# Performance work log

Measured on AMD Instinct MI355X. Metric: run time of the kernel, lower is better.

Reference implementation:

```python
import jax, jax.numpy as jnp
import numpy as np

EPS = 1e-5


def conv1d(x, w, b):
    # x: (B, C_in, S), w: (C_out, C_in, K), 'same' padding = K//2
    pad = w.shape[-1] // 2
    y = jax.lax.conv_general_dilated(
        x, w, window_strides=(1,), padding=[(pad, pad)],
        dimension_numbers=("NCH", "OIH", "NCH"))
    return y + b[None, :, None]


def layer_norm(x, g, b):
    m = jnp.mean(x, axis=-1, keepdims=True)
    v = jnp.var(x, axis=-1, keepdims=True)
    return (x - m) * jax.lax.rsqrt(v + EPS) * g + b


def duration_predict(x, conv1_w, conv1_b, conv2_w, conv2_b,
                     ln1_g, ln1_b, ln2_g, ln2_b, lin_w, lin_b):
    # x: (B, S, C)
    out = conv1d(jnp.swapaxes(x, -2, -1), conv1_w, conv1_b)          # (B, F, S)
    out = jax.nn.relu(layer_norm(jnp.swapaxes(out, -2, -1), ln1_g, ln1_b))  # (B, S, F)
    out = conv1d(jnp.swapaxes(out, -2, -1), conv2_w, conv2_b)        # (B, F, S)
    out = jax.nn.relu(layer_norm(jnp.swapaxes(out, -2, -1), ln2_g, ln2_b))  # (B, S, F)
    out = jax.nn.relu(out @ lin_w.T + lin_b)                          # (B, S, 1)
    return jnp.squeeze(out, -1)                                       # (B, S)


def setup_inputs() -> dict:
    key = jax.random.key(0)
    ks = jax.random.split(key, 6)
    B, S, C = 16, 1024, 256
    F_, K = 256, 3
    inp = {
        "x": jax.random.normal(ks[0], (B, S, C), dtype=jnp.float32),
        "target": jax.random.uniform(ks[1], (B, S), dtype=jnp.float32),
        "conv1_w": jax.random.normal(ks[2], (F_, C, K), dtype=jnp.float32) * 0.02,
        "conv1_b": jnp.zeros((F_,), dtype=jnp.float32),
        "conv2_w": jax.random.normal(ks[3], (F_, F_, K), dtype=jnp.float32) * 0.02,
        "conv2_b": jnp.zeros((F_,), dtype=jnp.float32),
        "ln1_g": jnp.ones((F_,), dtype=jnp.float32),
        "ln1_b": jnp.zeros((F_,), dtype=jnp.float32),
        "ln2_g": jnp.ones((F_,), dtype=jnp.float32),
        "ln2_b": jnp.zeros((F_,), dtype=jnp.float32),
        "lin_w": jax.random.normal(ks[4], (1, F_), dtype=jnp.float32) * 0.02,
        "lin_b": jnp.zeros((1,), dtype=jnp.float32),
    }
    return inp


def reference(x, target, conv1_w, conv1_b, conv2_w, conv2_b,
              ln1_g, ln1_b, ln2_g, ln2_b, lin_w, lin_b):
    reg_len = duration_predict(x, conv1_w, conv1_b, conv2_w, conv2_b,
                               ln1_g, ln1_b, ln2_g, ln2_b, lin_w, lin_b)
    # Faithful to the original: max_len uses exp(target), the mask uses round(target).
    # max_len is data-dependent -> computed from concrete target (host-side, like the original).
    max_len = int(np.round(float(jnp.max(jnp.sum(jnp.exp(target), axis=-1)))))
    d = jnp.round(target)                 # (B, S) integer-valued durations (banker's rounding, like Python round)
    fin = jnp.cumsum(d, axis=-1)          # (B, S) end offsets
    start = fin - d                       # (B, S) start offsets
    t = jnp.arange(max_len, dtype=target.dtype)  # (T,)
    mask = ((t[None, None, :] >= start[..., None]) &
            (t[None, None, :] < fin[..., None])).astype(x.dtype)  # (B, S, T)
    # x.transpose @ mask -> (B, C, T) -> transpose -> (B, T, C)
    expanded = jnp.einsum("bsc,bst->btc", x, mask)
    return expanded, reg_len
```

## Files before the change

kernel.cpp:

```cpp
#include <hip/hip_runtime.h>
#include <hip/hip_bf16.h>

using frag_ab = __attribute__((ext_vector_type(8))) short;
using frag_cd = __attribute__((ext_vector_type(4))) float;

#define SLEN 1024
#define CDIM 256
#define KTOT 768

static __device__ __forceinline__ short f2bf(float f) {
    __hip_bfloat16 h = __float2bfloat16(f);
    return *reinterpret_cast<short*>(&h);
}

__global__ __launch_bounds__(1024) void scan_scatter_kernel(
    const float* __restrict__ target, int* __restrict__ src, int T)
{
    const int b = blockIdx.x;
    const int tid = threadIdx.x;

    for (int i = tid; i < T; i += 1024) src[b * T + i] = -1;

    const float tv = target[b * SLEN + tid];
    const int d = (int)rintf(tv);

    const int lane = tid & 63;
    const int wid = tid >> 6;
    int v = d;
#pragma unroll
    for (int off = 1; off < 64; off <<= 1) {
        int n = __shfl_up(v, off);
        if (lane >= off) v += n;
    }
    __shared__ int waveSum[16];
    if (lane == 63) waveSum[wid] = v;
    __syncthreads();
    if (tid < 16) {
        int wv = waveSum[tid];
#pragma unroll
        for (int off = 1; off < 16; off <<= 1) {
            int n = __shfl_up(wv, off);
            if (tid >= off) wv += n;
        }
        waveSum[tid] = wv;
    }
    __syncthreads();
    const int fin = v + (wid > 0 ? waveSum[wid - 1] : 0);
    const int start = fin - d;
    for (int t = start; t < fin; ++t)
        if (t >= 0 && t < T) src[b * T + t] = tid;
}

__global__ __launch_bounds__(256) void expand_kernel(
    const float* __restrict__ x, const int* __restrict__ src,
    float* __restrict__ out, int T)
{
    const int row = blockIdx.x * 4 + (threadIdx.x >> 6);
    const int lane = threadIdx.x & 63;
    const int nrows = 16 * T;
    if (row >= nrows) return;
    const int b = row / T;
    const int s = src[row];
    float4 val = make_float4(0.f, 0.f, 0.f, 0.f);
    if (s >= 0)
        val = *(const float4*)(x + ((size_t)(b * SLEN + s)) * CDIM + lane * 4);
    *(float4*)(out + (size_t)row * CDIM + lane * 4) = val;
}

__global__ __launch_bounds__(256) void repack_w(
    const float* __restrict__ w, __hip_bfloat16* __restrict__ bt)
{
    const int f = blockIdx.y;
    const int K = blockIdx.x * 256 + threadIdx.x;
    const int k3 = K >> 8;
    const int c = K & 255;
    bt[f * KTOT + K] = __float2bfloat16(w[f * KTOT + c * 3 + k3]);
}

template <int MODE>
__global__ __launch_bounds__(512) void conv_mfma(
    const void* __restrict__ in_,
    const __hip_bfloat16* __restrict__ bt,
    const float* __restrict__ bias,
    const float* __restrict__ gamma,
    const float* __restrict__ beta,
    void* __restrict__ out_,
    const float* __restrict__ lw,
    const float* __restrict__ lb)
{
    __shared__ __align__(16) unsigned char ldsA[66 * 512];
    __shared__ float red[64][8][2];
    __shared__ float stats[64][2];

    const int tid = threadIdx.x;
    const int b = blockIdx.y;
    const int s0 = blockIdx.x * 64;

    if (MODE == 0) {
        const float* xin = (const float*)in_ + (size_t)b * SLEN * CDIM;
        for (int ii = tid; ii < 66 * 32; ii += 512) {
            const int r = ii >> 5, cc = ii & 31;
            const int s = s0 + r - 1;
            frag_ab v = {0, 0, 0, 0, 0, 0, 0, 0};
            if (s >= 0 && s < SLEN) {
                const float4* p = (const float4*)(xin + (size_t)s * CDIM + cc * 8);
                const float4 q0 = p[0], q1 = p[1];
                v[0] = f2bf(q0.x); v[1] = f2bf(q0.y); v[2] = f2bf(q0.z); v[3] = f2bf(q0.w);
                v[4] = f2bf(q1.x); v[5] = f2bf(q1.y); v[6] = f2bf(q1.z); v[7] = f2bf(q1.w);
            }
            *(frag_ab*)(ldsA + r * 512 + ((cc * 16) ^ ((r & 7) << 4))) = v;
        }
    } else {
        const __hip_bfloat16* yin = (const __hip_bfloat16*)in_ + (size_t)b * SLEN * CDIM;
        for (int ii = tid; ii < 66 * 32; ii += 512) {
            const int r = ii >> 5, cc = ii & 31;
            const int s = s0 + r - 1;
            frag_ab v = {0, 0, 0, 0, 0, 0, 0, 0};
            if (s >= 0 && s < SLEN)
                v = *(const frag_ab*)(yin + (size_t)s * CDIM + cc * 8);
            *(frag_ab*)(ldsA + r * 512 + ((cc * 16) ^ ((r & 7) << 4))) = v;
        }
    }
    __syncthreads();

    const int lane = tid & 63;
    const int wid = tid >> 6;
    const int l15 = lane & 15;
    const int lk = lane >> 4;
    const int fbase = wid * 32;

    frag_cd acc[4][2];
#pragma unroll
    for (int mf = 0; mf < 4; ++mf) {
        acc[mf][0] = {0.f, 0.f, 0.f, 0.f};
        acc[mf][1] = {0.f, 0.f, 0.f, 0.f};
    }

    const __hip_bfloat16* bt0 = bt + (size_t)(fbase + l15) * KTOT + lk * 8;
    const __hip_bfloat16* bt1 = bt0 + 16 * KTOT;

#pragma unroll
    for (int kk = 0; kk < 24; ++kk) {
        const int k3 = kk >> 3;
        const int colbyte = (kk & 7) * 64 + lk * 16;
        const frag_ab bb0 = *(const frag_ab*)(bt0 + kk * 32);
        const frag_ab bb1 = *(const frag_ab*)(bt1 + kk * 32);
        frag_ab a[4];
#pragma unroll
        for (int mf = 0; mf < 4; ++mf) {
            const int r = mf * 16 + l15 + k3;
            a[mf] = *(const frag_ab*)(ldsA + r * 512 + (colbyte ^ ((r & 7) << 4)));
        }
#pragma unroll
        for (int mf = 0; mf < 4; ++mf) {
            acc[mf][0] = __builtin_amdgcn_mfma_f32_16x16x32_bf16(a[mf], bb0, acc[mf][0], 0, 0, 0);
            acc[mf][1] = __builtin_amdgcn_mfma_f32_16x16x32_bf16(a[mf], bb1, acc[mf][1], 0, 0, 0);
        }
    }

    const float bias0 = bias[fbase + l15];
    const float bias1 = bias[fbase + 16 + l15];
#pragma unroll
    for (int mf = 0; mf < 4; ++mf) {
#pragma unroll
        for (int j = 0; j < 4; ++j) {
            acc[mf][0][j] += bias0;
            acc[mf][1][j] += bias1;
            float p = acc[mf][0][j] + acc[mf][1][j];
            float q = acc[mf][0][j] * acc[mf][0][j] + acc[mf][1][j] * acc[mf][1][j];
#pragma unroll
            for (int m = 1; m < 16; m <<= 1) {
                p += __shfl_xor(p, m);
                q += __shfl_xor(q, m);
            }
            if (l15 == 0) {
                const int row = mf * 16 + lk * 4 + j;
                red[row][wid][0] = p;
                red[row][wid][1] = q;
            }
        }
    }
    __syncthreads();
    if (tid < 64) {
        float s = 0.f, q = 0.f;
#pragma unroll
        for (int wv = 0; wv < 8; ++wv) { s += red[tid][wv][0]; q += red[tid][wv][1]; }
        const float mean = s * (1.f / 256.f);
        const float var = q * (1.f / 256.f) - mean * mean;
        stats[tid][0] = mean;
        stats[tid][1] = rsqrtf(var + 1e-5f);
    }
    __syncthreads();

    const float g0 = gamma[fbase + l15], g1 = gamma[fbase + 16 + l15];
    const float be0 = beta[fbase + l15], be1 = beta[fbase + 16 + l15];

    if (MODE == 0) {
#pragma unroll
        for (int mf = 0; mf < 4; ++mf) {
#pragma unroll
            for (int j = 0; j < 4; ++j) {
                const int row = mf * 16 + lk * 4 + j;
                const float mean = stats[row][0], rs = stats[row][1];
                const float v0 = fmaxf((acc[mf][0][j] - mean) * rs * g0 + be0, 0.f);
                const float v1 = fmaxf((acc[mf][1][j] - mean) * rs * g1 + be1, 0.f);
                *(short*)(ldsA + row * 512 + (fbase + l15) * 2) = f2bf(v0);
                *(short*)(ldsA + row * 512 + (fbase + 16 + l15) * 2) = f2bf(v1);
            }
        }
        __syncthreads();
        __hip_bfloat16* yout = (__hip_bfloat16*)out_ + ((size_t)b * SLEN + s0) * CDIM;
        for (int ii = tid; ii < 64 * 32; ii += 512) {
            const int r = ii >> 5, cc = ii & 31;
            *(frag_ab*)(yout + (size_t)r * CDIM + cc * 8) =
                *(const frag_ab*)(ldsA + r * 512 + cc * 16);
        }
    } else {
        const float lw0 = lw[fbase + l15], lw1 = lw[fbase + 16 + l15];
#pragma unroll
        for (int mf = 0; mf < 4; ++mf) {
#pragma unroll
            for (int j = 0; j < 4; ++j) {
                const int row = mf * 16 + lk * 4 + j;
                const float mean = stats[row][0], rs = stats[row][1];
                const float v0 = fmaxf((acc[mf][0][j] - mean) * rs * g0 + be0, 0.f);
                const float v1 = fmaxf((acc[mf][1][j] - mean) * rs * g1 + be1, 0.f);
                float p = v0 * lw0 + v1 * lw1;
#pragma unroll
                for (int m = 1; m < 16; m <<= 1) p += __shfl_xor(p, m);
                if (l15 == 0) red[row][wid][0] = p;
            }
        }
        __syncthreads();
        if (tid < 64) {
            float s = 0.f;
#pragma unroll
            for (int wv = 0; wv < 8; ++wv) s += red[tid][wv][0];
            ((float*)out_)[b * SLEN + s0 + tid] = fmaxf(s + lb[0], 0.f);
        }
    }
}

extern "C" void kernel_launch(void* const* d_in, const int* in_sizes, int n_in,
                              void* d_out, int out_size, void* d_ws, size_t ws_size,
                              hipStream_t stream)
{
    const float* x       = (const float*)d_in[0];
    const float* target  = (const float*)d_in[1];
    const float* conv1_w = (const float*)d_in[2];
    const float* conv1_b = (const float*)d_in[3];
    const float* conv2_w = (const float*)d_in[4];
    const float* conv2_b = (const float*)d_in[5];
    const float* ln1_g   = (const float*)d_in[6];
    const float* ln1_b   = (const float*)d_in[7];
    const float* ln2_g   = (const float*)d_in[8];
    const float* ln2_b   = (const float*)d_in[9];
    const float* lin_w   = (const float*)d_in[10];
    const float* lin_b   = (const float*)d_in[11];

    const int B = 16, S = 1024, C = 256;
    const int T = (out_size - B * S) / (B * C);

    float* expanded = (float*)d_out;
    float* reg_len  = (float*)d_out + (size_t)B * T * C;

    unsigned char* ws = (unsigned char*)d_ws;
    __hip_bfloat16* y1  = (__hip_bfloat16*)ws;
    __hip_bfloat16* bt1 = (__hip_bfloat16*)(ws + 8388608);
    __hip_bfloat16* bt2 = (__hip_bfloat16*)(ws + 8388608 + 393216);
    int* src = (int*)(ws + 8388608 + 2 * 393216);

    scan_scatter_kernel<<<B, 1024, 0, stream>>>(target, src, T);
    repack_w<<<dim3(3, 256), 256, 0, stream>>>(conv1_w, bt1);
    repack_w<<<dim3(3, 256), 256, 0, stream>>>(conv2_w, bt2);

    conv_mfma<0><<<dim3(16, 16), 512, 0, stream>>>(
        x, bt1, conv1_b, ln1_g, ln1_b, y1, nullptr, nullptr);

    expand_kernel<<<(B * T + 3) / 4, 256, 0, stream>>>(x, src, expanded, T);

    conv_mfma<1><<<dim3(16, 16), 512, 0, stream>>>(
        y1, bt2, conv2_b, ln2_g, ln2_b, reg_len, lin_w, lin_b);
}
```

Before: 62.91 us.

## Fuse both conv+layernorm stages into one kernel with halo recompute

Merges the two conv_mfma launches into a single kernel. Each block loads a 68-row x tile (two halo rows each side), computes conv1+LN1+ReLU for 66 rows into LDS, then runs conv2+LN2+linear directly from LDS. This removes the bf16 intermediate round trip through global memory and one kernel launch, at the cost of recomputing the halo rows, more LDS per block and more registers. The two weight-repack launches are also merged into one.

New measurement: 57.07 us. -9.3%, faster.

```diff
diff --git a/kernel.cpp b/kernel.cpp
--- a/kernel.cpp
+++ b/kernel.cpp
@@ -67,59 +67,50 @@
     *(float4*)(out + (size_t)row * CDIM + lane * 4) = val;
 }
 
-__global__ __launch_bounds__(256) void repack_w(
-    const float* __restrict__ w, __hip_bfloat16* __restrict__ bt)
+__global__ __launch_bounds__(256) void repack_w2(
+    const float* __restrict__ w1, __hip_bfloat16* __restrict__ bt1,
+    const float* __restrict__ w2, __hip_bfloat16* __restrict__ bt2)
 {
     const int f = blockIdx.y;
-    const int K = blockIdx.x * 256 + threadIdx.x;
+    const int which = blockIdx.x / 3;
+    const int K = (blockIdx.x % 3) * 256 + threadIdx.x;
     const int k3 = K >> 8;
     const int c = K & 255;
+    const float* w = which ? w2 : w1;
+    __hip_bfloat16* bt = which ? bt2 : bt1;
     bt[f * KTOT + K] = __float2bfloat16(w[f * KTOT + c * 3 + k3]);
 }
 
-template <int MODE>
-__global__ __launch_bounds__(512) void conv_mfma(
-    const void* __restrict__ in_,
-    const __hip_bfloat16* __restrict__ bt,
-    const float* __restrict__ bias,
-    const float* __restrict__ gamma,
-    const float* __restrict__ beta,
-    void* __restrict__ out_,
-    const float* __restrict__ lw,
-    const float* __restrict__ lb)
-{
-    __shared__ __align__(16) unsigned char ldsA[66 * 512];
-    __shared__ float red[64][8][2];
-    __shared__ float stats[64][2];
+__global__ __launch_bounds__(512) void fused_conv(
+    const float* __restrict__ x,
+    const __hip_bfloat16* __restrict__ bt1,
+    const __hip_bfloat16* __restrict__ bt2,
+    const float* __restrict__ cb1, const float* __restrict__ g1, const float* __restrict__ be1,
+    const float* __restrict__ cb2, const float* __restrict__ g2, const float* __restrict__ be2,
+    const float* __restrict__ lw, const float* __restrict__ lb,
+    float* __restrict__ reg_len)
+{
+    __shared__ __align__(16) unsigned char xt[82 * 512];
+    __shared__ __align__(16) unsigned char yt[66 * 512];
+    __shared__ float red[66][8][2];
+    __shared__ float stats[66][2];
 
     const int tid = threadIdx.x;
     const int b = blockIdx.y;
     const int s0 = blockIdx.x * 64;
 
-    if (MODE == 0) {
-        const float* xin = (const float*)in_ + (size_t)b * SLEN * CDIM;
-        for (int ii = tid; ii < 66 * 32; ii += 512) {
-            const int r = ii >> 5, cc = ii & 31;
-            const int s = s0 + r - 1;
-            frag_ab v = {0, 0, 0, 0, 0, 0, 0, 0};
-            if (s >= 0 && s < SLEN) {
-                const float4* p = (const float4*)(xin + (size_t)s * CDIM + cc * 8);
-                const float4 q0 = p[0], q1 = p[1];
-                v[0] = f2bf(q0.x); v[1] = f2bf(q0.y); v[2] = f2bf(q0.z); v[3] = f2bf(q0.w);
-                v[4] = f2bf(q1.x); v[5] = f2bf(q1.y); v[6] = f2bf(q1.z); v[7] = f2bf(q1.w);
-            }
-            *(frag_ab*)(ldsA + r * 512 + ((cc * 16) ^ ((r & 7) << 4))) = v;
-        }
-    } else {
-        const __hip_bfloat16* yin = (const __hip_bfloat16*)in_ + (size_t)b * SLEN * CDIM;
-        for (int ii = tid; ii < 66 * 32; ii += 512) {
-            const int r = ii >> 5, cc = ii & 31;
-            const int s = s0 + r - 1;
-            frag_ab v = {0, 0, 0, 0, 0, 0, 0, 0};
-            if (s >= 0 && s < SLEN)
-                v = *(const frag_ab*)(yin + (size_t)s * CDIM + cc * 8);
-            *(frag_ab*)(ldsA + r * 512 + ((cc * 16) ^ ((r & 7) << 4))) = v;
-        }
+    const float* xin = x + (size_t)b * SLEN * CDIM;
+    for (int ii = tid; ii < 68 * 32; ii += 512) {
+        const int r = ii >> 5, cc = ii & 31;
+        const int s = s0 - 2 + r;
+        frag_ab v = {0, 0, 0, 0, 0, 0, 0, 0};
+        if (s >= 0 && s < SLEN) {
+            const float4* p = (const float4*)(xin + (size_t)s * CDIM + cc * 8);
+            const float4 q0 = p[0], q1 = p[1];
+            v[0] = f2bf(q0.x); v[1] = f2bf(q0.y); v[2] = f2bf(q0.z); v[3] = f2bf(q0.w);
+            v[4] = f2bf(q1.x); v[5] = f2bf(q1.y); v[6] = f2bf(q1.z); v[7] = f2bf(q1.w);
+        }
+        *(frag_ab*)(xt + r * 512 + ((cc * 16) ^ ((r & 7) << 4))) = v;
     }
     __syncthreads();
 
@@ -129,59 +120,62 @@
     const int lk = lane >> 4;
     const int fbase = wid * 32;
 
-    frag_cd acc[4][2];
-#pragma unroll
-    for (int mf = 0; mf < 4; ++mf) {
-        acc[mf][0] = {0.f, 0.f, 0.f, 0.f};
-        acc[mf][1] = {0.f, 0.f, 0.f, 0.f};
-    }
-
-    const __hip_bfloat16* bt0 = bt + (size_t)(fbase + l15) * KTOT + lk * 8;
-    const __hip_bfloat16* bt1 = bt0 + 16 * KTOT;
-
-#pragma unroll
-    for (int kk = 0; kk < 24; ++kk) {
-        const int k3 = kk >> 3;
-        const int colbyte = (kk & 7) * 64 + lk * 16;
-        const frag_ab bb0 = *(const frag_ab*)(bt0 + kk * 32);
-        const frag_ab bb1 = *(const frag_ab*)(bt1 + kk * 32);
-        frag_ab a[4];
-#pragma unroll
-        for (int mf = 0; mf < 4; ++mf) {
-            const int r = mf * 16 + l15 + k3;
-            a[mf] = *(const frag_ab*)(ldsA + r * 512 + (colbyte ^ ((r & 7) << 4)));
-        }
-#pragma unroll
-        for (int mf = 0; mf < 4; ++mf) {
-            acc[mf][0] = __builtin_amdgcn_mfma_f32_16x16x32_bf16(a[mf], bb0, acc[mf][0], 0, 0, 0);
-            acc[mf][1] = __builtin_amdgcn_mfma_f32_16x16x32_bf16(a[mf], bb1, acc[mf][1], 0, 0, 0);
-        }
-    }
-
-    const float bias0 = bias[fbase + l15];
-    const float bias1 = bias[fbase + 16 + l15];
-#pragma unroll
-    for (int mf = 0; mf < 4; ++mf) {
-#pragma unroll
-        for (int j = 0; j < 4; ++j) {
-            acc[mf][0][j] += bias0;
-            acc[mf][1][j] += bias1;
-            float p = acc[mf][0][j] + acc[mf][1][j];
-            float q = acc[mf][0][j] * acc[mf][0][j] + acc[mf][1][j] * acc[mf][1][j];
-#pragma unroll
-            for (int m = 1; m < 16; m <<= 1) {
-                p += __shfl_xor(p, m);
-                q += __shfl_xor(q, m);
-            }
-            if (l15 == 0) {
-                const int row = mf * 16 + lk * 4 + j;
-                red[row][wid][0] = p;
-                red[row][wid][1] = q;
-            }
-        }
-    }
-    __syncthreads();
-    if (tid < 64) {
+    frag_cd acc1[5][2];
+#pragma unroll
+    for (int mf = 0; mf < 5; ++mf) {
+        acc1[mf][0] = {0.f, 0.f, 0.f, 0.f};
+        acc1[mf][1] = {0.f, 0.f, 0.f, 0.f};
+    }
+    {
+        const __hip_bfloat16* p0 = bt1 + (size_t)(fbase + l15) * KTOT + lk * 8;
+        const __hip_bfloat16* p1 = p0 + 16 * KTOT;
+#pragma unroll
+        for (int kk = 0; kk < 24; ++kk) {
+            const int k3 = kk >> 3;
+            const int colbyte = (kk & 7) * 64 + lk * 16;
+            const frag_ab bb0 = *(const frag_ab*)(p0 + kk * 32);
+            const frag_ab bb1 = *(const frag_ab*)(p1 + kk * 32);
+            frag_ab a[5];
+#pragma unroll
+            for (int mf = 0; mf < 5; ++mf) {
+                const int r = mf * 16 + l15 + k3;
+                a[mf] = *(const frag_ab*)(xt + r * 512 + (colbyte ^ ((r & 7) << 4)));
+            }
+#pragma unroll
+            for (int mf = 0; mf < 5; ++mf) {
+                acc1[mf][0] = __builtin_amdgcn_mfma_f32_16x16x32_bf16(a[mf], bb0, acc1[mf][0], 0, 0, 0);
+                acc1[mf][1] = __builtin_amdgcn_mfma_f32_16x16x32_bf16(a[mf], bb1, acc1[mf][1], 0, 0, 0);
+            }
+        }
+    }
+
+    {
+        const float bias0 = cb1[fbase + l15];
+        const float bias1 = cb1[fbase + 16 + l15];
+#pragma unroll
+        for (int mf = 0; mf < 5; ++mf) {
+#pragma unroll
+            for (int j = 0; j < 4; ++j) {
+                acc1[mf][0][j] += bias0;
+                acc1[mf][1][j] += bias1;
+                float p = acc1[mf][0][j] + acc1[mf][1][j];
+                float q = acc1[mf][0][j] * acc1[mf][0][j] + acc1[mf][1][j] * acc1[mf][1][j];
+#pragma unroll
+                for (int m = 1; m < 16; m <<= 1) {
+                    p += __shfl_xor(p, m);
+                    q += __shfl_xor(q, m);
+                }
+                const bool valid = (mf < 4) || (lk == 0 && j < 2);
+                if (l15 == 0 && valid) {
+                    const int yr = mf * 16 + lk * 4 + j;
+                    red[yr][wid][0] = p;
+                    red[yr][wid][1] = q;
+                }
+            }
+        }
+    }
+    __syncthreads();
+    if (tid < 66) {
         float s = 0.f, q = 0.f;
 #pragma unroll
         for (int wv = 0; wv < 8; ++wv) { s += red[tid][wv][0]; q += red[tid][wv][1]; }
@@ -192,52 +186,130 @@
     }
     __syncthreads();
 
-    const float g0 = gamma[fbase + l15], g1 = gamma[fbase + 16 + l15];
-    const float be0 = beta[fbase + l15], be1 = beta[fbase + 16 + l15];
-
-    if (MODE == 0) {
+    {
+        const float ga0 = g1[fbase + l15], ga1 = g1[fbase + 16 + l15];
+        const float bb0 = be1[fbase + l15], bb1 = be1[fbase + 16 + l15];
+        const int c0b = (fbase + l15) * 2;
+        const int c1b = (fbase + 16 + l15) * 2;
+#pragma unroll
+        for (int mf = 0; mf < 5; ++mf) {
+#pragma unroll
+            for (int j = 0; j < 4; ++j) {
+                const bool valid = (mf < 4) || (lk == 0 && j < 2);
+                if (valid) {
+                    const int yr = mf * 16 + lk * 4 + j;
+                    const float mean = stats[yr][0], rs = stats[yr][1];
+                    const float v0 = fmaxf((acc1[mf][0][j] - mean) * rs * ga0 + bb0, 0.f);
+                    const float v1 = fmaxf((acc1[mf][1][j] - mean) * rs * ga1 + bb1, 0.f);
+                    const int sw = (yr & 7) << 4;
+                    *(short*)(yt + yr * 512 + (c0b ^ sw)) = f2bf(v0);
+                    *(short*)(yt + yr * 512 + (c1b ^ sw)) = f2bf(v1);
+                }
+            }
+        }
+    }
+    __syncthreads();
+    if (blockIdx.x == 0 && tid < 32) {
+        frag_ab z = {0, 0, 0, 0, 0, 0, 0, 0};
+        *(frag_ab*)(yt + (tid * 16)) = z;
+    }
+    if (blockIdx.x == 15 && tid >= 64 && tid < 96) {
+        frag_ab z = {0, 0, 0, 0, 0, 0, 0, 0};
+        const int cc = tid - 64;
+        *(frag_ab*)(yt + 65 * 512 + ((cc * 16) ^ ((65 & 7) << 4))) = z;
+    }
+    __syncthreads();
+
+    frag_cd acc2[4][2];
+#pragma unroll
+    for (int mf = 0; mf < 4; ++mf) {
+        acc2[mf][0] = {0.f, 0.f, 0.f, 0.f};
+        acc2[mf][1] = {0.f, 0.f, 0.f, 0.f};
+    }
+    {
+        const __hip_bfloat16* p0 = bt2 + (size_t)(fbase + l15) * KTOT + lk * 8;
+        const __hip_bfloat16* p1 = p0 + 16 * KTOT;
+#pragma unroll
+        for (int kk = 0; kk < 24; ++kk) {
+            const int k3 = kk >> 3;
+            const int colbyte = (kk & 7) * 64 + lk * 16;
+            const frag_ab bb0 = *(const frag_ab*)(p0 + kk * 32);
+            const frag_ab bb1 = *(const frag_ab*)(p1 + kk * 32);
+            frag_ab a[4];
+#pragma unroll
+            for (int mf = 0; mf < 4; ++mf) {
+                const int r = mf * 16 + l15 + k3;
+                a[mf] = *(const frag_ab*)(yt + r * 512 + (colbyte ^ ((r & 7) << 4)));
+            }
+#pragma unroll
+            for (int mf = 0; mf < 4; ++mf) {
+                acc2[mf][0] = __builtin_amdgcn_mfma_f32_16x16x32_bf16(a[mf], bb0, acc2[mf][0], 0, 0, 0);
+                acc2[mf][1] = __builtin_amdgcn_mfma_f32_16x16x32_bf16(a[mf], bb1, acc2[mf][1], 0, 0, 0);
+            }
+        }
+    }
+
+    {
+        const float bias0 = cb2[fbase + l15];
+        const float bias1 = cb2[fbase + 16 + l15];
+#pragma unroll
+        for (int mf = 0; mf < 4; ++mf) {
+#pragma unroll
+            for (int j = 0; j < 4; ++j) {
+                acc2[mf][0][j] += bias0;
+                acc2[mf][1][j] += bias1;
+                float p = acc2[mf][0][j] + acc2[mf][1][j];
+                float q = acc2[mf][0][j] * acc2[mf][0][j] + acc2[mf][1][j] * acc2[mf][1][j];
+#pragma unroll
+                for (int m = 1; m < 16; m <<= 1) {
+                    p += __shfl_xor(p, m);
+                    q += __shfl_xor(q, m);
+                }
+                if (l15 == 0) {
+                    const int row = mf * 16 + lk * 4 + j;
+                    red[row][wid][0] = p;
+                    red[row][wid][1] = q;
+                }
+            }
+        }
+    }
+    __syncthreads();
+    if (tid < 64) {
+        float s = 0.f, q = 0.f;
+#pragma unroll
+        for (int wv = 0; wv < 8; ++wv) { s += red[tid][wv][0]; q += red[tid][wv][1]; }
+        const float mean = s * (1.f / 256.f);
+        const float var = q * (1.f / 256.f) - mean * mean;
+        stats[tid][0] = mean;
+        stats[tid][1] = rsqrtf(var + 1e-5f);
+    }
+    __syncthreads();
+
+    {
+        const float ga0 = g2[fbase + l15], ga1 = g2[fbase + 16 + l15];
+        const float bb0 = be2[fbase + l15], bb1 = be2[fbase + 16 + l15];
+        const float lw0 = lw[fbase + l15], lw1 = lw[fbase + 16 + l15];
 #pragma unroll
         for (int mf = 0; mf < 4; ++mf) {
 #pragma unroll
             for (int j = 0; j < 4; ++j) {
                 const int row = mf * 16 + lk * 4 + j;
                 const float mean = stats[row][0], rs = stats[row][1];
-                const float v0 = fmaxf((acc[mf][0][j] - mean) * rs * g0 + be0, 0.f);
-                const float v1 = fmaxf((acc[mf][1][j] - mean) * rs * g1 + be1, 0.f);
-                *(short*)(ldsA + row * 512 + (fbase + l15) * 2) = f2bf(v0);
-                *(short*)(ldsA + row * 512 + (fbase + 16 + l15) * 2) = f2bf(v1);
-            }
-        }
-        __syncthreads();
-        __hip_bfloat16* yout = (__hip_bfloat16*)out_ + ((size_t)b * SLEN + s0) * CDIM;
-        for (int ii = tid; ii < 64 * 32; ii += 512) {
-            const int r = ii >> 5, cc = ii & 31;
-            *(frag_ab*)(yout + (size_t)r * CDIM + cc * 8) =
-                *(const frag_ab*)(ldsA + r * 512 + cc * 16);
-        }
-    } else {
-        const float lw0 = lw[fbase + l15], lw1 = lw[fbase + 16 + l15];
-#pragma unroll
-        for (int mf = 0; mf < 4; ++mf) {
-#pragma unroll
-            for (int j = 0; j < 4; ++j) {
-                const int row = mf * 16 + lk * 4 + j;
-                const float mean = stats[row][0], rs = stats[row][1];
-                const float v0 = fmaxf((acc[mf][0][j] - mean) * rs * g0 + be0, 0.f);
-                const float v1 = fmaxf((acc[mf][1][j] - mean) * rs * g1 + be1, 0.f);
+                const float v0 = fmaxf((acc2[mf][0][j] - mean) * rs * ga0 + bb0, 0.f);
+                const float v1 = fmaxf((acc2[mf][1][j] - mean) * rs * ga1 + bb1, 0.f);
                 float p = v0 * lw0 + v1 * lw1;
 #pragma unroll
                 for (int m = 1; m < 16; m <<= 1) p += __shfl_xor(p, m);
                 if (l15 == 0) red[row][wid][0] = p;
             }
         }
-        __syncthreads();
-        if (tid < 64) {
-            float s = 0.f;
-#pragma unroll
-            for (int wv = 0; wv < 8; ++wv) s += red[tid][wv][0];
-            ((float*)out_)[b * SLEN + s0 + tid] = fmaxf(s + lb[0], 0.f);
-        }
+    }
+    __syncthreads();
+    if (tid < 64) {
+        float s = 0.f;
+#pragma unroll
+        for (int wv = 0; wv < 8; ++wv) s += red[tid][wv][0];
+        reg_len[b * SLEN + s0 + tid] = fmaxf(s + lb[0], 0.f);
     }
 }
 
@@ -265,20 +337,16 @@
     float* reg_len  = (float*)d_out + (size_t)B * T * C;
 
     unsigned char* ws = (unsigned char*)d_ws;
-    __hip_bfloat16* y1  = (__hip_bfloat16*)ws;
-    __hip_bfloat16* bt1 = (__hip_bfloat16*)(ws + 8388608);
-    __hip_bfloat16* bt2 = (__hip_bfloat16*)(ws + 8388608 + 393216);
-    int* src = (int*)(ws + 8388608 + 2 * 393216);
+    __hip_bfloat16* bt1 = (__hip_bfloat16*)ws;
+    __hip_bfloat16* bt2 = (__hip_bfloat16*)(ws + 393216);
+    int* src = (int*)(ws + 2 * 393216);
 
     scan_scatter_kernel<<<B, 1024, 0, stream>>>(target, src, T);
-    repack_w<<<dim3(3, 256), 256, 0, stream>>>(conv1_w, bt1);
-    repack_w<<<dim3(3, 256), 256, 0, stream>>>(conv2_w, bt2);
-
-    conv_mfma<0><<<dim3(16, 16), 512, 0, stream>>>(
-        x, bt1, conv1_b, ln1_g, ln1_b, y1, nullptr, nullptr);
+    repack_w2<<<dim3(6, 256), 256, 0, stream>>>(conv1_w, bt1, conv2_w, bt2);
+
+    fused_conv<<<dim3(16, 16), 512, 0, stream>>>(
+        x, bt1, bt2, conv1_b, ln1_g, ln1_b, conv2_b, ln2_g, ln2_b,
+        lin_w, lin_b, reg_len);
 
     expand_kernel<<<(B * T + 3) / 4, 256, 0, stream>>>(x, src, expanded, T);
-
-    conv_mfma<1><<<dim3(16, 16), 512, 0, stream>>>(
-        y1, bt2, conv2_b, ln2_g, ln2_b, reg_len, lin_w, lin_b);
-}
+}
```
